# Kernel optimization log

Hardware: AMD Instinct MI355X
Metric: run time of the kernel (lower is better)

Reference implementation:

```python
import jax, jax.numpy as jnp
import numpy as np

B, T, N, F_IN = 2, 4, 1024, 256
H, N_HIDDEN = 8, 128
SLOPE = 0.2
NEG_INF = -9e16


def setup_inputs() -> dict:
    key = jax.random.key(0)
    k1, k2, k3, k4 = jax.random.split(key, 4)
    h = jax.random.normal(k1, (B, T, N, F_IN), dtype=jnp.float32)
    adj_mat = jax.random.randint(k2, (N, N), 0, 2, dtype=jnp.int32)
    W = jax.random.normal(k3, (F_IN, H * N_HIDDEN), dtype=jnp.float32) * 0.05
    a = jax.random.normal(k4, (H, 2 * N_HIDDEN, 1), dtype=jnp.float32) * 0.05
    return {"h": h, "adj_mat": adj_mat, "W": W, "a": a}


def reference(h, adj_mat, W, a):
    b, t, n, _ = h.shape
    # linear transform: [B,T,N,F_in] @ [F_in, H*nh] -> [B,T,N,H*nh]
    ht = jnp.einsum('btjs,sh->btjh', h, W)
    # dropout is identity in eval mode
    ht = ht.reshape(b, t, n, H, N_HIDDEN).transpose(0, 1, 3, 2, 4)  # [B,T,H,N,nh]
    # additive attention scores
    a_src = a[:, :N_HIDDEN, :]   # [H, nh, 1]
    a_tgt = a[:, N_HIDDEN:, :]   # [H, nh, 1]
    src = jnp.einsum('bthnd,hdo->bthno', ht, a_src)  # [B,T,H,N,1]
    tgt = jnp.einsum('bthnd,hdo->bthno', ht, a_tgt)  # [B,T,H,N,1]
    e = src + jnp.swapaxes(tgt, -1, -2)              # [B,T,H,N,N]
    e = jnp.where(e >= 0, e, SLOPE * e)              # LeakyReLU
    e = jnp.where(adj_mat > 0, e, jnp.float32(NEG_INF))
    attention = jax.nn.softmax(e, axis=-1)
    # weighted aggregation: [B,T,H,N,N] @ [B,T,H,N,nh]
    h_prime = jnp.einsum('bthij,bthjd->bthid', attention, ht)
    # concat=False branch: mean over dim 0 (batch), as in the source
    return h_prime.mean(axis=0)  # [T,H,N,nh]
```

## Files before the change

### kernel.cpp

```cpp
#include <hip/hip_runtime.h>
#include <cstddef>
#include <cstdint>

#define B_ 2
#define T_ 4
#define N_ 1024
#define FIN_ 256
#define H_ 8
#define D_ 128
#define L2E_ 1.4426950408889634f

typedef __attribute__((ext_vector_type(8))) short short8;
typedef __attribute__((ext_vector_type(4))) float f32x4;
typedef __attribute__((ext_vector_type(2))) float f32x2;

#define MFMA16(A, B, C) __builtin_amdgcn_mfma_f32_16x16x32_bf16((A), (B), (C), 0, 0, 0)

__device__ __forceinline__ unsigned short f2bf(float f) {
    uint32_t u = __float_as_uint(f);
    uint32_t r = (u + 0x7fffu + ((u >> 16) & 1u)) >> 16;
    return (unsigned short)r;
}

__device__ __forceinline__ uint32_t cvt_pk_bf16(float lo, float hi) {
    uint32_t r;
    asm volatile("v_cvt_pk_bf16_f32 %0, %1, %2" : "=v"(r) : "v"(lo), "v"(hi));
    return r;
}

__device__ __forceinline__ float fexp2(float x) {
#if __has_builtin(__builtin_amdgcn_exp2f)
    return __builtin_amdgcn_exp2f(x);
#else
    float r;
    asm("v_exp_f32 %0, %1" : "=v"(r) : "v"(x));
    return r;
#endif
}

__device__ __forceinline__ void load_lds16(const unsigned short* g, unsigned short* l) {
    __builtin_amdgcn_global_load_lds(
        (const __attribute__((address_space(1))) uint32_t*)g,
        (__attribute__((address_space(3))) uint32_t*)l, 16, 0, 0);
}

__global__ __launch_bounds__(256) void k_prep(const float* __restrict__ W,
                                              const float* __restrict__ a,
                                              unsigned short* __restrict__ Wt_bf,
                                              float* __restrict__ wa) {
    __shared__ float wl[64][68];
    const int bid = blockIdx.x, tid = threadIdx.x;
    if (bid < 64) {
        const int tb  = bid;
        const int hk0 = (tb >> 2) * 64;
        const int s0  = (tb & 3) * 64;
        {
            const int r  = tid >> 2;
            const int c0 = (tid & 3) * 16;
            #pragma unroll
            for (int k = 0; k < 4; ++k)
                *(float4*)&wl[r][c0 + k * 4] =
                    *(const float4*)(W + (size_t)(s0 + r) * (H_ * D_) + hk0 + c0 + k * 4);
        }
        __syncthreads();
        {
            const int r2 = tid >> 2;
            const int c2 = (tid & 3) * 16;
            unsigned short ob[16];
            #pragma unroll
            for (int k = 0; k < 16; ++k) ob[k] = f2bf(wl[c2 + k][r2]);
            unsigned short* dst = Wt_bf + (size_t)(hk0 + r2) * FIN_ + s0 + c2;
            *(uint4*)(dst)     = *(uint4*)&ob[0];
            *(uint4*)(dst + 8) = *(uint4*)&ob[8];
        }
    } else {
        const int o    = (bid - 64) * 256 + tid;
        const int head = o >> 9;
        const int st   = (o >> 8) & 1;
        const int s    = o & 255;
        const float* wr = W + (size_t)s * (H_ * D_) + head * D_;
        const float* ar = a + head * 256 + st * 128;
        float sum = 0.f;
        #pragma unroll
        for (int d = 0; d < 128; d += 4) {
            const float4 wv = *(const float4*)(wr + d);
            const float4 av = *(const float4*)(ar + d);
            sum += wv.x * av.x + wv.y * av.y + wv.z * av.z + wv.w * av.w;
        }
        wa[s * 16 + head * 2 + st] = sum;
    }
}

__global__ __launch_bounds__(256, 2) void k_gemm_sp(const float* __restrict__ h,
                                                    const unsigned short* __restrict__ Wt_bf,
                                                    const float* __restrict__ wa,
                                                    const int* __restrict__ adj,
                                                    unsigned short* __restrict__ htT,
                                                    float* __restrict__ s1,
                                                    float* __restrict__ t1,
                                                    uint32_t* __restrict__ adjm) {
    __shared__ __align__(16) char smem[24576];
    const int bid = blockIdx.x, tid = threadIdx.x;
    if (bid < 1024) {
        unsigned short* a_lds = (unsigned short*)smem;
        unsigned short* b_lds = (unsigned short*)(smem + 16384);
        const int xcd  = bid & 7;
        const int slot = bid >> 3;
        const int gid  = xcd * 8 + (slot >> 4);
        const int bt   = gid >> 3;
        const int n0   = (gid & 7) * 128;
        const int hk0  = (slot & 15) * 64;
        const int w = tid >> 6, lane = tid & 63;
        const int row16 = lane & 15, kgrp = lane >> 4;
        const int kswz = (kgrp ^ ((row16 >> 1) & 3)) * 8;
        const int ar  = tid >> 1;
        const int akh = tid & 1;
        const int asub = ar >> 4, arow = ar & 15;
        const int ax = (arow >> 1) & 3;
        const int aslot0 = ((akh * 2) ^ ax) * 8;
        const int aslot1 = ((akh * 2 + 1) ^ ax) * 8;
        const float* ga = h + ((size_t)bt * N_ + n0 + ar) * FIN_ + akh * 16;
        unsigned short* aw_ = a_lds + asub * 512 + arow * 32;
        const int brow = lane >> 2;
        const int bsb  = (lane & 3) ^ ((lane >> 3) & 3);
        const unsigned short* gb = Wt_bf + (size_t)(hk0 + w * 16 + brow) * FIN_ + bsb * 8;
        unsigned short* bw_ = b_lds + w * 512 + (size_t)lane * 8;

        float4 rf0, rf1, rf2, rf3;

#define LOADA(KS) {                                                            \
        const float* g = ga + (KS) * 32;                                       \
        rf0 = *(const float4*)(g);      rf1 = *(const float4*)(g + 4);         \
        rf2 = *(const float4*)(g + 8);  rf3 = *(const float4*)(g + 12); }

#define WRITEA(BUF) {                                                          \
        uint4 o0, o1;                                                          \
        o0.x = cvt_pk_bf16(rf0.x, rf0.y); o0.y = cvt_pk_bf16(rf0.z, rf0.w);    \
        o0.z = cvt_pk_bf16(rf1.x, rf1.y); o0.w = cvt_pk_bf16(rf1.z, rf1.w);    \
        o1.x = cvt_pk_bf16(rf2.x, rf2.y); o1.y = cvt_pk_bf16(rf2.z, rf2.w);    \
        o1.z = cvt_pk_bf16(rf3.x, rf3.y); o1.w = cvt_pk_bf16(rf3.z, rf3.w);    \
        unsigned short* ad = aw_ + (BUF) * 4096;                               \
        *(uint4*)(ad + aslot0) = o0;                                           \
        *(uint4*)(ad + aslot1) = o1; }

#define COMPK(BUF) {                                                           \
        const unsigned short* ab = a_lds + (BUF) * 4096;                       \
        const short8 bfv = *(const short8*)(b_lds + (BUF) * 2048 + w * 512 + row16 * 32 + kswz); \
        _Pragma("unroll")                                                      \
        for (int nt = 0; nt < 8; ++nt) {                                       \
            const short8 afv = *(const short8*)(ab + nt * 512 + row16 * 32 + kswz); \
            acc[nt] = MFMA16(afv, bfv, acc[nt]);                               \
        } }

        f32x4 acc[8];
        #pragma unroll
        for (int nt = 0; nt < 8; ++nt) acc[nt] = (f32x4){0.f, 0.f, 0.f, 0.f};

        LOADA(0)
        WRITEA(0)
        load_lds16(gb, bw_);
        LOADA(1)
        asm volatile("s_waitcnt vmcnt(4) lgkmcnt(0)" ::: "memory");
        __builtin_amdgcn_s_barrier();

        for (int ks = 0; ks < 8; ++ks) {
            const int cur = ks & 1;
            WRITEA(cur ^ 1)
            load_lds16(gb + ((ks + 1) & 7) * 32, bw_ + (cur ^ 1) * 2048);
            LOADA((ks + 2) & 7)
            COMPK(cur)
            asm volatile("s_waitcnt vmcnt(4) lgkmcnt(0)" ::: "memory");
            __builtin_amdgcn_s_barrier();
        }
#undef LOADA
#undef WRITEA
#undef COMPK
        const int hk   = hk0 + w * 16 + row16;
        const int head = hk >> 7;
        const int d    = hk & 127;
        unsigned short* ob = htT + ((size_t)(bt * H_ + head) * D_ + d) * N_;
        #pragma unroll
        for (int nt = 0; nt < 8; ++nt) {
            ushort4 v;
            v.x = f2bf(acc[nt][0]); v.y = f2bf(acc[nt][1]);
            v.z = f2bf(acc[nt][2]); v.w = f2bf(acc[nt][3]);
            *(ushort4*)(ob + n0 + nt * 16 + kgrp * 4) = v;
        }
    } else if (bid < 1152) {
        float (*was)[16] = (float(*)[16])smem;
        {
            const int f = tid * 16;
            #pragma unroll
            for (int k = 0; k < 4; ++k)
                *(float4*)&was[f >> 4][k * 4] = *(const float4*)(wa + f + k * 4);
        }
        __syncthreads();
        const int r = tid >> 2, q = tid & 3;
        const int R = (bid - 1024) * 64 + r;
        const float* hrow = h + (size_t)R * FIN_ + q * 64;
        float acc[16];
        #pragma unroll
        for (int o = 0; o < 16; ++o) acc[o] = 0.f;
        for (int k = 0; k < 64; k += 4) {
            const float4 hv = *(const float4*)(hrow + k);
            const int s = q * 64 + k;
            #pragma unroll
            for (int kk = 0; kk < 4; ++kk) {
                const float hs = (kk == 0) ? hv.x : (kk == 1) ? hv.y : (kk == 2) ? hv.z : hv.w;
                #pragma unroll
                for (int o = 0; o < 16; ++o) acc[o] += hs * was[s + kk][o];
            }
        }
        #pragma unroll
        for (int o = 0; o < 16; ++o) {
            acc[o] += __shfl_xor(acc[o], 1);
            acc[o] += __shfl_xor(acc[o], 2);
        }
        const int bt = R >> 10, n = R & 1023;
        #pragma unroll
        for (int k = 0; k < 4; ++k) {
            const int o = q * 4 + k;
            const int head = o >> 1;
            const size_t idx = ((size_t)(bt * H_ + head)) * N_ + n;
            const float v = acc[o] * L2E_;
            if (o & 1) t1[idx] = v;
            else       s1[idx] = v;
        }
    } else {
        const int w0 = ((bid - 1152) * 256 + tid) * 4;
        const int4 p0 = *(const int4*)(adj + (size_t)w0 * 2);
        const int4 p1 = *(const int4*)(adj + (size_t)w0 * 2 + 4);
        uint4 m;
        m.x = (p0.x > 0 ? 0xFFFFu : 0u) | (p0.y > 0 ? 0xFFFF0000u : 0u);
        m.y = (p0.z > 0 ? 0xFFFFu : 0u) | (p0.w > 0 ? 0xFFFF0000u : 0u);
        m.z = (p1.x > 0 ? 0xFFFFu : 0u) | (p1.y > 0 ? 0xFFFF0000u : 0u);
        m.w = (p1.z > 0 ? 0xFFFFu : 0u) | (p1.w > 0 ? 0xFFFF0000u : 0u);
        *(uint4*)(adjm + w0) = m;
    }
}

struct SC {
    float4 a1l, a1h;
    uint4  m4A, m4B;
};

__global__ __launch_bounds__(256, 2) void k_attn(const unsigned short* __restrict__ htT,
                                                 const float* __restrict__ s1,
                                                 const float* __restrict__ t1,
                                                 const uint32_t* __restrict__ adjm,
                                                 float* __restrict__ out) {
    __shared__ __align__(16) char smem[65536];
    unsigned short* stg = (unsigned short*)smem;
    const int xcd  = blockIdx.x & 7;
    const int slot = blockIdx.x >> 3;
    const int th   = xcd * 4 + (slot >> 4);
    const int i0   = (slot & 15) * 64;
    const int tid = threadIdx.x;
    const int w = tid >> 6, lane = tid & 63;
    const int b = w & 1, isub = w >> 1;
    const int row16 = lane & 15, kgrp = lane >> 4, jrel = kgrp * 8;
    const int kswz = (kgrp ^ ((row16 >> 1) & 3)) * 8;
    const int bth = b * (T_ * H_) + th;
    const int iA  = i0 + isub * 32 + row16;
    const int iB  = iA + 16;
    const float s1A = s1[(size_t)bth * N_ + iA];
    const float s1B = s1[(size_t)bth * N_ + iB];
    const f32x2 s1A2 = {s1A, s1A}, s1B2 = {s1B, s1B};
    const f32x2 c02  = {0.2f, 0.2f};
    const float* t1b = t1 + (size_t)bth * N_;
    const uint32_t* amA = adjm + (size_t)iA * (N_ / 2);
    const uint32_t* amB = adjm + (size_t)iB * (N_ / 2);

    const int sd0 = lane >> 2;
    const int sj  = ((lane & 3) ^ ((sd0 >> 1) & 3)) * 8;
    const unsigned short* gstg = htT + ((size_t)bth * D_ + sd0) * N_ + sj;
    unsigned short* lstg = stg + (size_t)w * 8192 + (size_t)lane * 8;

#define STAGE(BUF, T32) {                                        \
        const unsigned short* gs = gstg + (size_t)(T32) * 32;    \
        unsigned short* ls = lstg + (BUF) * 4096;                \
        load_lds16(gs,            ls);                           \
        load_lds16(gs + 16 * N_,  ls + 512);                     \
        load_lds16(gs + 32 * N_,  ls + 1024);                    \
        load_lds16(gs + 48 * N_,  ls + 1536);                    \
        load_lds16(gs + 64 * N_,  ls + 2048);                    \
        load_lds16(gs + 80 * N_,  ls + 2560);                    \
        load_lds16(gs + 96 * N_,  ls + 3072);                    \
        load_lds16(gs + 112 * N_, ls + 3584); }

#define LOADSC(S, T32) {                                         \
        S.a1l = *(const float4*)(t1b + (T32) * 32 + jrel);       \
        S.a1h = *(const float4*)(t1b + (T32) * 32 + jrel + 4);   \
        S.m4A = *(const uint4*)(amA + (T32) * 16 + kgrp * 4);    \
        S.m4B = *(const uint4*)(amB + (T32) * 16 + kgrp * 4); }

    f32x4 accA[8], accB[8];
    #pragma unroll
    for (int nt = 0; nt < 8; ++nt) {
        accA[nt] = (f32x4){0.f, 0.f, 0.f, 0.f};
        accB[nt] = (f32x4){0.f, 0.f, 0.f, 0.f};
    }
    f32x4 daccA = (f32x4){0.f, 0.f, 0.f, 0.f};
    f32x4 daccB = (f32x4){0.f, 0.f, 0.f, 0.f};
    short8 ones8;
    {
        const short ov = (row16 == 0) ? (short)0x3F80 : (short)0;
        #pragma unroll
        for (int e = 0; e < 8; ++e) ones8[e] = ov;
    }
    const unsigned short* rdbase = stg + (size_t)w * 8192 + row16 * 32 + kswz;

    SC sc;

#define SUBP(BUFIDX, TNEXT)                                                    \
    {                                                                          \
        const f32x2 tq[4] = {{sc.a1l.x, sc.a1l.y}, {sc.a1l.z, sc.a1l.w},       \
                             {sc.a1h.x, sc.a1h.y}, {sc.a1h.z, sc.a1h.w}};      \
        const uint32_t mAw[4] = {sc.m4A.x, sc.m4A.y, sc.m4A.z, sc.m4A.w};      \
        const uint32_t mBw[4] = {sc.m4B.x, sc.m4B.y, sc.m4B.z, sc.m4B.w};      \
        short8 afA, afB;                                                       \
        _Pragma("unroll")                                                      \
        for (int p = 0; p < 4; ++p) {                                          \
            const f32x2 eA  = s1A2 + tq[p];                                    \
            const f32x2 eB  = s1B2 + tq[p];                                    \
            const f32x2 eA2 = eA * c02;                                        \
            const f32x2 eB2 = eB * c02;                                        \
            const float wA0 = fexp2(fmaxf(eA[0], eA2[0]));                     \
            const float wA1 = fexp2(fmaxf(eA[1], eA2[1]));                     \
            const float wB0 = fexp2(fmaxf(eB[0], eB2[0]));                     \
            const float wB1 = fexp2(fmaxf(eB[1], eB2[1]));                     \
            ((uint32_t*)&afA)[p] = cvt_pk_bf16(wA0, wA1) & mAw[p];             \
            ((uint32_t*)&afB)[p] = cvt_pk_bf16(wB0, wB1) & mBw[p];             \
        }                                                                      \
        LOADSC(sc, (TNEXT))                                                    \
        const unsigned short* rb = rdbase + (BUFIDX) * 4096;                   \
        short8 bfr[8];                                                         \
        _Pragma("unroll")                                                      \
        for (int nt = 0; nt < 8; ++nt) bfr[nt] = *(const short8*)(rb + nt * 512); \
        _Pragma("unroll")                                                      \
        for (int nt = 0; nt < 8; ++nt) {                                       \
            accA[nt] = MFMA16(afA, bfr[nt], accA[nt]);                         \
            accB[nt] = MFMA16(afB, bfr[nt], accB[nt]);                         \
        }                                                                      \
        daccA = MFMA16(afA, ones8, daccA);                                     \
        daccB = MFMA16(afB, ones8, daccB);                                     \
    }

    STAGE(0, 0)
    LOADSC(sc, 0)

    for (int t = 0; t < 32; ++t) {
        STAGE((t + 1) & 1, (t + 1) & 31)
        asm volatile("s_waitcnt vmcnt(12)" ::: "memory");
        SUBP(t & 1, (t + 1) & 31)
    }
#undef SUBP
#undef LOADSC
#undef STAGE

    float ivA[4], ivB[4];
    #pragma unroll
    for (int r = 0; r < 4; ++r) {
        ivA[r] = __shfl(1.0f / daccA[r], kgrp * 16);
        ivB[r] = __shfl(1.0f / daccB[r], kgrp * 16);
    }

    __syncthreads();
    float* comb = (float*)smem;
    if (b == 1) {
        #pragma unroll
        for (int nt = 0; nt < 8; ++nt)
            #pragma unroll
            for (int r = 0; r < 4; ++r) {
                const int il = isub * 32 + kgrp * 4 + r;
                const int d  = nt * 16 + row16;
                comb[il * 128 + d]        = accA[nt][r] * ivA[r];
                comb[(il + 16) * 128 + d] = accB[nt][r] * ivB[r];
            }
    }
    __syncthreads();
    if (b == 0) {
        #pragma unroll
        for (int nt = 0; nt < 8; ++nt)
            #pragma unroll
            for (int r = 0; r < 4; ++r) {
                const int il = isub * 32 + kgrp * 4 + r;
                const int d  = nt * 16 + row16;
                out[((size_t)th * N_ + i0 + il) * D_ + d] =
                    0.5f * (accA[nt][r] * ivA[r] + comb[il * 128 + d]);
                out[((size_t)th * N_ + i0 + il + 16) * D_ + d] =
                    0.5f * (accB[nt][r] * ivB[r] + comb[(il + 16) * 128 + d]);
            }
    }
}

extern "C" void kernel_launch(void* const* d_in, const int* in_sizes, int n_in,
                              void* d_out, int out_size, void* d_ws, size_t ws_size,
                              hipStream_t stream) {
    const float* h   = (const float*)d_in[0];
    const int*   adj = (const int*)d_in[1];
    const float* W   = (const float*)d_in[2];
    const float* a   = (const float*)d_in[3];
    float* out = (float*)d_out;

    char* p = (char*)d_ws;
    unsigned short* htT = (unsigned short*)p;  p += (size_t)B_ * T_ * H_ * D_ * N_ * 2;
    float* s1 = (float*)p;                     p += (size_t)B_ * T_ * H_ * N_ * 4;
    float* t1 = (float*)p;                     p += (size_t)B_ * T_ * H_ * N_ * 4;
    uint32_t* adjm = (uint32_t*)p;             p += (size_t)N_ * N_ / 2 * 4;
    unsigned short* Wt_bf = (unsigned short*)p;p += (size_t)(H_ * D_) * FIN_ * 2;
    float* wa = (float*)p;

    k_prep<<<dim3(80), dim3(256), 0, stream>>>(W, a, Wt_bf, wa);
    k_gemm_sp<<<dim3(1664), dim3(256), 0, stream>>>(h, Wt_bf, wa, adj, htT, s1, t1, adjm);
    k_attn<<<dim3(512), dim3(256), 0, stream>>>(htT, s1, t1, adjm, out);
}
```

Measured before the change: 78.86 us.

## Share staged V tiles across waves and halve rows per block in attention kernel

The attention kernel now handles 32 query rows per block instead of 64, and the grid doubles to 1024 blocks. Each wave computes one 16-row MFMA tile instead of two. Instead of every wave staging its own full copy of the ht tile, the four waves cooperatively stage one tile per batch into shared LDS, which halves LDS use to 32KB and removes redundant global loads. This adds a workgroup barrier every iteration and reduces per-wave MFMA work per staged byte, in exchange for lower register pressure, more blocks and higher occupancy.

```diff
diff --git a/kernel.cpp b/kernel.cpp
--- a/kernel.cpp
+++ b/kernel.cpp
@@ -241,7 +241,7 @@
 
 struct SC {
     float4 a1l, a1h;
-    uint4  m4A, m4B;
+    uint4  m4A;
 };
 
 __global__ __launch_bounds__(256, 2) void k_attn(const unsigned short* __restrict__ htT,
@@ -249,66 +249,55 @@
                                                  const float* __restrict__ t1,
                                                  const uint32_t* __restrict__ adjm,
                                                  float* __restrict__ out) {
-    __shared__ __align__(16) char smem[65536];
+    __shared__ __align__(16) char smem[32768];
     unsigned short* stg = (unsigned short*)smem;
     const int xcd  = blockIdx.x & 7;
     const int slot = blockIdx.x >> 3;
-    const int th   = xcd * 4 + (slot >> 4);
-    const int i0   = (slot & 15) * 64;
+    const int th   = xcd * 4 + (slot >> 5);
+    const int i0   = (slot & 31) * 32;
     const int tid = threadIdx.x;
     const int w = tid >> 6, lane = tid & 63;
-    const int b = w & 1, isub = w >> 1;
+    const int b = w & 1, half = w >> 1;
     const int row16 = lane & 15, kgrp = lane >> 4, jrel = kgrp * 8;
     const int kswz = (kgrp ^ ((row16 >> 1) & 3)) * 8;
     const int bth = b * (T_ * H_) + th;
-    const int iA  = i0 + isub * 32 + row16;
-    const int iB  = iA + 16;
+    const int iA  = i0 + half * 16 + row16;
     const float s1A = s1[(size_t)bth * N_ + iA];
-    const float s1B = s1[(size_t)bth * N_ + iB];
-    const f32x2 s1A2 = {s1A, s1A}, s1B2 = {s1B, s1B};
+    const f32x2 s1A2 = {s1A, s1A};
     const f32x2 c02  = {0.2f, 0.2f};
     const float* t1b = t1 + (size_t)bth * N_;
     const uint32_t* amA = adjm + (size_t)iA * (N_ / 2);
-    const uint32_t* amB = adjm + (size_t)iB * (N_ / 2);
-
-    const int sd0 = lane >> 2;
-    const int sj  = ((lane & 3) ^ ((sd0 >> 1) & 3)) * 8;
-    const unsigned short* gstg = htT + ((size_t)bth * D_ + sd0) * N_ + sj;
-    unsigned short* lstg = stg + (size_t)w * 8192 + (size_t)lane * 8;
+
+    const int sb  = w >> 1;
+    const int sd0 = (w & 1) * 64 + (lane >> 2);
+    const int sj  = ((lane & 3) ^ ((lane >> 3) & 3)) * 8;
+    const unsigned short* gstg = htT + ((size_t)(sb * (T_ * H_) + th) * D_ + sd0) * N_ + sj;
+    unsigned short* lstg = stg + (size_t)w * 2048 + (size_t)lane * 8;
 
 #define STAGE(BUF, T32) {                                        \
         const unsigned short* gs = gstg + (size_t)(T32) * 32;    \
-        unsigned short* ls = lstg + (BUF) * 4096;                \
-        load_lds16(gs,            ls);                           \
-        load_lds16(gs + 16 * N_,  ls + 512);                     \
-        load_lds16(gs + 32 * N_,  ls + 1024);                    \
-        load_lds16(gs + 48 * N_,  ls + 1536);                    \
-        load_lds16(gs + 64 * N_,  ls + 2048);                    \
-        load_lds16(gs + 80 * N_,  ls + 2560);                    \
-        load_lds16(gs + 96 * N_,  ls + 3072);                    \
-        load_lds16(gs + 112 * N_, ls + 3584); }
+        unsigned short* ls = lstg + (BUF) * 8192;                \
+        load_lds16(gs,           ls);                            \
+        load_lds16(gs + 16 * N_, ls + 512);                      \
+        load_lds16(gs + 32 * N_, ls + 1024);                     \
+        load_lds16(gs + 48 * N_, ls + 1536); }
 
 #define LOADSC(S, T32) {                                         \
         S.a1l = *(const float4*)(t1b + (T32) * 32 + jrel);       \
         S.a1h = *(const float4*)(t1b + (T32) * 32 + jrel + 4);   \
-        S.m4A = *(const uint4*)(amA + (T32) * 16 + kgrp * 4);    \
-        S.m4B = *(const uint4*)(amB + (T32) * 16 + kgrp * 4); }
-
-    f32x4 accA[8], accB[8];
+        S.m4A = *(const uint4*)(amA + (T32) * 16 + kgrp * 4); }
+
+    f32x4 acc[8];
     #pragma unroll
-    for (int nt = 0; nt < 8; ++nt) {
-        accA[nt] = (f32x4){0.f, 0.f, 0.f, 0.f};
-        accB[nt] = (f32x4){0.f, 0.f, 0.f, 0.f};
-    }
-    f32x4 daccA = (f32x4){0.f, 0.f, 0.f, 0.f};
-    f32x4 daccB = (f32x4){0.f, 0.f, 0.f, 0.f};
+    for (int nt = 0; nt < 8; ++nt) acc[nt] = (f32x4){0.f, 0.f, 0.f, 0.f};
+    f32x4 dacc = (f32x4){0.f, 0.f, 0.f, 0.f};
     short8 ones8;
     {
         const short ov = (row16 == 0) ? (short)0x3F80 : (short)0;
         #pragma unroll
         for (int e = 0; e < 8; ++e) ones8[e] = ov;
     }
-    const unsigned short* rdbase = stg + (size_t)w * 8192 + row16 * 32 + kswz;
+    const unsigned short* rdbase = stg + b * 4096 + row16 * 32 + kswz;
 
     SC sc;
 
@@ -317,53 +306,43 @@
         const f32x2 tq[4] = {{sc.a1l.x, sc.a1l.y}, {sc.a1l.z, sc.a1l.w},       \
                              {sc.a1h.x, sc.a1h.y}, {sc.a1h.z, sc.a1h.w}};      \
         const uint32_t mAw[4] = {sc.m4A.x, sc.m4A.y, sc.m4A.z, sc.m4A.w};      \
-        const uint32_t mBw[4] = {sc.m4B.x, sc.m4B.y, sc.m4B.z, sc.m4B.w};      \
-        short8 afA, afB;                                                       \
+        short8 af;                                                             \
         _Pragma("unroll")                                                      \
         for (int p = 0; p < 4; ++p) {                                          \
             const f32x2 eA  = s1A2 + tq[p];                                    \
-            const f32x2 eB  = s1B2 + tq[p];                                    \
             const f32x2 eA2 = eA * c02;                                        \
-            const f32x2 eB2 = eB * c02;                                        \
             const float wA0 = fexp2(fmaxf(eA[0], eA2[0]));                     \
             const float wA1 = fexp2(fmaxf(eA[1], eA2[1]));                     \
-            const float wB0 = fexp2(fmaxf(eB[0], eB2[0]));                     \
-            const float wB1 = fexp2(fmaxf(eB[1], eB2[1]));                     \
-            ((uint32_t*)&afA)[p] = cvt_pk_bf16(wA0, wA1) & mAw[p];             \
-            ((uint32_t*)&afB)[p] = cvt_pk_bf16(wB0, wB1) & mBw[p];             \
+            ((uint32_t*)&af)[p] = cvt_pk_bf16(wA0, wA1) & mAw[p];              \
         }                                                                      \
         LOADSC(sc, (TNEXT))                                                    \
-        const unsigned short* rb = rdbase + (BUFIDX) * 4096;                   \
+        const unsigned short* rb = rdbase + (BUFIDX) * 8192;                   \
         short8 bfr[8];                                                         \
         _Pragma("unroll")                                                      \
         for (int nt = 0; nt < 8; ++nt) bfr[nt] = *(const short8*)(rb + nt * 512); \
         _Pragma("unroll")                                                      \
-        for (int nt = 0; nt < 8; ++nt) {                                       \
-            accA[nt] = MFMA16(afA, bfr[nt], accA[nt]);                         \
-            accB[nt] = MFMA16(afB, bfr[nt], accB[nt]);                         \
-        }                                                                      \
-        daccA = MFMA16(afA, ones8, daccA);                                     \
-        daccB = MFMA16(afB, ones8, daccB);                                     \
+        for (int nt = 0; nt < 8; ++nt) acc[nt] = MFMA16(af, bfr[nt], acc[nt]); \
+        dacc = MFMA16(af, ones8, dacc);                                        \
     }
 
     STAGE(0, 0)
     LOADSC(sc, 0)
 
     for (int t = 0; t < 32; ++t) {
+        asm volatile("s_waitcnt vmcnt(3)" ::: "memory");
+        __builtin_amdgcn_s_barrier();
+        asm volatile("" ::: "memory");
         STAGE((t + 1) & 1, (t + 1) & 31)
-        asm volatile("s_waitcnt vmcnt(12)" ::: "memory");
         SUBP(t & 1, (t + 1) & 31)
     }
 #undef SUBP
 #undef LOADSC
 #undef STAGE
 
-    float ivA[4], ivB[4];
+    float iv[4];
     #pragma unroll
-    for (int r = 0; r < 4; ++r) {
-        ivA[r] = __shfl(1.0f / daccA[r], kgrp * 16);
-        ivB[r] = __shfl(1.0f / daccB[r], kgrp * 16);
-    }
+    for (int r = 0; r < 4; ++r)
+        iv[r] = __shfl(1.0f / dacc[r], kgrp * 16);
 
     __syncthreads();
     float* comb = (float*)smem;
@@ -372,10 +351,9 @@
         for (int nt = 0; nt < 8; ++nt)
             #pragma unroll
             for (int r = 0; r < 4; ++r) {
-                const int il = isub * 32 + kgrp * 4 + r;
+                const int il = half * 16 + kgrp * 4 + r;
                 const int d  = nt * 16 + row16;
-                comb[il * 128 + d]        = accA[nt][r] * ivA[r];
-                comb[(il + 16) * 128 + d] = accB[nt][r] * ivB[r];
+                comb[il * 128 + d] = acc[nt][r] * iv[r];
             }
     }
     __syncthreads();
@@ -384,12 +362,10 @@
         for (int nt = 0; nt < 8; ++nt)
             #pragma unroll
             for (int r = 0; r < 4; ++r) {
-                const int il = isub * 32 + kgrp * 4 + r;
+                const int il = half * 16 + kgrp * 4 + r;
                 const int d  = nt * 16 + row16;
                 out[((size_t)th * N_ + i0 + il) * D_ + d] =
-                    0.5f * (accA[nt][r] * ivA[r] + comb[il * 128 + d]);
-                out[((size_t)th * N_ + i0 + il + 16) * D_ + d] =
-                    0.5f * (accB[nt][r] * ivB[r] + comb[(il + 16) * 128 + d]);
+                    0.5f * (acc[nt][r] * iv[r] + comb[il * 128 + d]);
             }
     }
 }
@@ -413,5 +389,5 @@
 
     k_prep<<<dim3(80), dim3(256), 0, stream>>>(W, a, Wt_bf, wa);
     k_gemm_sp<<<dim3(1664), dim3(256), 0, stream>>>(h, Wt_bf, wa, adj, htT, s1, t1, adjm);
-    k_attn<<<dim3(512), dim3(256), 0, stream>>>(htT, s1, t1, adjm, out);
-}
+    k_attn<<<dim3(1024), dim3(256), 0, stream>>>(htT, s1, t1, adjm, out);
+}
```

New measurement: 84.05 us. +6.6%, slower.
